# Optimization experiments

Hardware: AMD Instinct MI355X
Metric: run time of the kernel (lower is better)

Reference implementation:

```python
import jax, jax.numpy as jnp
import numpy as np
import math

B, N, D, L, H, FF, T = 8, 256, 384, 6, 8, 1536, 4
Dh = D // H  # 48, divisible by 6 for 3D rotary
N_M1 = T + 1 + 2 * N  # learn tokens + state + hand + head
S = 2 * N_M1


def rotary_pe_3d(x, coords):
    # x: [B,H,S,Dh], coords: [B,S,3]. Split head dim into 3 axis chunks,
    # apply standard RoPE per axis using the continuous coordinate as position.
    dh = x.shape[-1]
    d = dh // 3
    half = d // 2
    inv_freq = 1.0 / (10000.0 ** (jnp.arange(half, dtype=x.dtype) / half))
    outs = []
    for a in range(3):
        xa = x[..., a * d:(a + 1) * d]
        ang = coords[..., a][:, None, :, None] * inv_freq  # [B,1,S,half]
        c, s = jnp.cos(ang), jnp.sin(ang)
        x1, x2 = xa[..., :half], xa[..., half:]
        outs.append(jnp.concatenate([x1 * c - x2 * s, x1 * s + x2 * c], axis=-1))
    return jnp.concatenate(outs, axis=-1)


def layernorm(x, g, b):
    m = jnp.mean(x, axis=-1, keepdims=True)
    v = jnp.var(x, axis=-1, keepdims=True)
    return (x - m) * jax.lax.rsqrt(v + 1e-5) * g + b


def transformer_layer(src, coords_src, mask, Wq, bq, Wk, bk, Wv, bv, Wo, bo, W1, b1, W2, b2, g1, be1, g2, be2):
    Bsz, Ss, _ = src.shape
    q = jnp.einsum('bsd,od->bso', src, Wq) + bq
    k = jnp.einsum('bsd,od->bso', src, Wk) + bk
    v = jnp.einsum('bsd,od->bso', src, Wv) + bv
    q = q.reshape(Bsz, Ss, H, Dh).transpose(0, 2, 1, 3)
    k = k.reshape(Bsz, Ss, H, Dh).transpose(0, 2, 1, 3)
    v = v.reshape(Bsz, Ss, H, Dh).transpose(0, 2, 1, 3)
    q = rotary_pe_3d(q, coords_src)
    k = rotary_pe_3d(k, coords_src)
    scores = jnp.einsum('bhqd,bhkd->bhqk', q, k) / math.sqrt(Dh)
    scores = jnp.where(mask[None, None, :, :], -jnp.inf, scores)
    attn = jnp.einsum('bhqk,bhkd->bhqd', jax.nn.softmax(scores, axis=-1), v)
    attn = attn.transpose(0, 2, 1, 3).reshape(Bsz, Ss, D)
    attn = jnp.einsum('bsd,od->bso', attn, Wo) + bo
    src2 = layernorm(src + attn, g1, be1)
    ff = jnp.einsum('bsf,of->bso', jax.nn.gelu(jnp.einsum('bsd,fd->bsf', src2, W1) + b1, approximate=False), W2) + b2
    return layernorm(src2 + ff, g2, be2)


def setup_inputs() -> dict:
    key = jax.random.key(0)
    ks = jax.random.split(key, 32)
    rnd = lambda i, shape, scale=1.0: (jax.random.normal(ks[i], shape, dtype=jnp.float32) * scale)
    inp = {
        'hand_token_t': rnd(0, (B, N, D)),
        'head_token_t': rnd(1, (B, N, D)),
        'hand_token_m1': rnd(2, (B, N, D)),
        'head_token_m1': rnd(3, (B, N, D)),
        'coords_hand_t': rnd(4, (B, N, 3)),
        'coords_head_t': rnd(5, (B, N, 3)),
        'coords_hand_m1': rnd(6, (B, N, 3)),
        'coords_head_m1': rnd(7, (B, N, 3)),
        'state_t': rnd(8, (B, D)),
        'state_m1': rnd(9, (B, D)),
        'trans_head_t': rnd(10, (B, 3)),
        'trans_head_m1': rnd(11, (B, 3)),
        'tokens_m1': rnd(12, (1, T, D), 0.02),
        'tokens_t': rnd(13, (1, T, D), 0.02),
        'Wq': rnd(14, (L, D, D), 0.02), 'bq': jnp.zeros((L, D), jnp.float32),
        'Wk': rnd(15, (L, D, D), 0.02), 'bk': jnp.zeros((L, D), jnp.float32),
        'Wv': rnd(16, (L, D, D), 0.02), 'bv': jnp.zeros((L, D), jnp.float32),
        'Wo': rnd(17, (L, D, D), 0.02), 'bo': jnp.zeros((L, D), jnp.float32),
        'W1': rnd(18, (L, FF, D), 0.02), 'b1': jnp.zeros((L, FF), jnp.float32),
        'W2': rnd(19, (L, D, FF), 0.02), 'b2': jnp.zeros((L, D), jnp.float32),
        'g1': jnp.ones((L, D), jnp.float32), 'be1': jnp.zeros((L, D), jnp.float32),
        'g2': jnp.ones((L, D), jnp.float32), 'be2': jnp.zeros((L, D), jnp.float32),
    }
    return inp


def reference(hand_token_t, head_token_t, hand_token_m1, head_token_m1,
              coords_hand_t, coords_head_t, coords_hand_m1, coords_head_m1,
              state_t, state_m1, trans_head_t, trans_head_m1,
              tokens_m1, tokens_t, Wq, bq, Wk, bk, Wv, bv, Wo, bo,
              W1, b1, W2, b2, g1, be1, g2, be2):
    # Build token sequence: [state_m1, hand_m1, head_m1, learn_m1, state_t, hand_t, head_t, learn_t]
    tok_m1 = jnp.broadcast_to(tokens_m1, (B, T, D))
    tok_t = jnp.broadcast_to(tokens_t, (B, T, D))
    coord_m1 = jnp.broadcast_to(trans_head_m1[:, None, :], (B, T, 3))
    coord_t = jnp.broadcast_to(trans_head_t[:, None, :], (B, T, 3))
    src = jnp.concatenate([
        state_m1[:, None, :], hand_token_m1, head_token_m1, tok_m1,
        state_t[:, None, :], hand_token_t, head_token_t, tok_t], axis=1)
    coords_src = jnp.concatenate([
        trans_head_m1[:, None, :], coords_hand_m1, coords_head_m1, coord_m1,
        trans_head_t[:, None, :], coords_hand_t, coords_head_t, coord_t], axis=1)
    # block-causal mask: m1 block cannot attend to t block
    mask = jnp.zeros((S, S), dtype=bool).at[:N_M1, N_M1:].set(True)
    for i in range(L):
        src = transformer_layer(src, coords_src, mask,
                                Wq[i], bq[i], Wk[i], bk[i], Wv[i], bv[i], Wo[i], bo[i],
                                W1[i], b1[i], W2[i], b2[i], g1[i], be1[i], g2[i], be2[i])
    return src[:, -T:, :]
```

## Files before the change

kernel.cpp:

```cpp
#include <hip/hip_runtime.h>
#include <hip/hip_bf16.h>
#include <math.h>

#define BB 8
#define NN 256
#define DD 384
#define LL 6
#define HH 8
#define FFD 1536
#define TT 4
#define DH 48
#define NM1 517
#define SS 1034
#define SSP 1088
#define MROWS (BB*SS)
#define NQKV 1152
#define QSCALE2 (0.14433756729740643f * 1.4426950408889634f)

typedef unsigned short u16;
typedef unsigned int u32;
typedef short bf8 __attribute__((ext_vector_type(8)));
typedef float f32x4 __attribute__((ext_vector_type(4)));

__device__ __forceinline__ u16 f2bf(float f) {
  __hip_bfloat16 h = __float2bfloat16(f);
  return *reinterpret_cast<u16*>(&h);
}
__device__ __forceinline__ float bf2f(u16 u) {
  __hip_bfloat16 h;
  *reinterpret_cast<u16*>(&h) = u;
  return __bfloat162float(h);
}
__device__ __forceinline__ float max3f(float a, float b, float c) {
  return fmaxf(fmaxf(a, b), c);
}
__device__ __forceinline__ void async16(void* lds, const void* g) {
  __builtin_amdgcn_global_load_lds(
      (const __attribute__((address_space(1))) unsigned int*)g,
      (__attribute__((address_space(3))) unsigned int*)lds, 16, 0, 0);
}

__global__ void build_src(const float* __restrict__ hand_t, const float* __restrict__ head_t,
                          const float* __restrict__ hand_m1, const float* __restrict__ head_m1,
                          const float* __restrict__ state_t, const float* __restrict__ state_m1,
                          const float* __restrict__ tok_m1, const float* __restrict__ tok_t,
                          float* __restrict__ src, u16* __restrict__ srcb) {
  int idx = blockIdx.x * 256 + threadIdx.x;
  if (idx >= BB * SS * DD) return;
  int d = idx % DD;
  int bs = idx / DD;
  int s = bs % SS;
  int b = bs / SS;
  float val;
  if (s == 0)               val = state_m1[b * DD + d];
  else if (s <= NN)         val = hand_m1[((size_t)(b * NN + (s - 1))) * DD + d];
  else if (s <= 2 * NN)     val = head_m1[((size_t)(b * NN + (s - 1 - NN))) * DD + d];
  else if (s <= 2 * NN + TT) val = tok_m1[(s - (2 * NN + 1)) * DD + d];
  else if (s == NM1)        val = state_t[b * DD + d];
  else if (s <= NM1 + NN)   val = hand_t[((size_t)(b * NN + (s - NM1 - 1))) * DD + d];
  else if (s <= NM1 + 2 * NN) val = head_t[((size_t)(b * NN + (s - NM1 - 1 - NN))) * DD + d];
  else                      val = tok_t[(s - (NM1 + 2 * NN + 1)) * DD + d];
  src[idx] = val;
  srcb[idx] = f2bf(val);
}

__global__ void build_coords(const float* __restrict__ c_hand_t, const float* __restrict__ c_head_t,
                             const float* __restrict__ c_hand_m1, const float* __restrict__ c_head_m1,
                             const float* __restrict__ tr_t, const float* __restrict__ tr_m1,
                             float* __restrict__ coords) {
  int idx = blockIdx.x * 256 + threadIdx.x;
  if (idx >= BB * SS * 3) return;
  int a = idx % 3;
  int bs = idx / 3;
  int s = bs % SS;
  int b = bs / SS;
  float val;
  if (s == 0)               val = tr_m1[b * 3 + a];
  else if (s <= NN)         val = c_hand_m1[(b * NN + (s - 1)) * 3 + a];
  else if (s <= 2 * NN)     val = c_head_m1[(b * NN + (s - 1 - NN)) * 3 + a];
  else if (s <= 2 * NN + TT) val = tr_m1[b * 3 + a];
  else if (s == NM1)        val = tr_t[b * 3 + a];
  else if (s <= NM1 + NN)   val = c_hand_t[(b * NN + (s - NM1 - 1)) * 3 + a];
  else if (s <= NM1 + 2 * NN) val = c_head_t[(b * NN + (s - NM1 - 1 - NN)) * 3 + a];
  else                      val = tr_t[b * 3 + a];
  coords[idx] = val;
}

__global__ void build_trig(const float* __restrict__ coords, float2* __restrict__ trig) {
  int idx = blockIdx.x * 256 + threadIdx.x;
  if (idx >= BB * SS * 24) return;
  int i = idx & 7;
  int axis = (idx >> 3) % 3;
  int bs = idx / 24;
  float cv = coords[bs * 3 + axis];
  float inv = expf(-(float)i * 1.1512925464970229f);
  float ang = cv * inv;
  trig[idx] = make_float2(cosf(ang), sinf(ang));
}

__global__ void cvt_bf(const float* __restrict__ in, u16* __restrict__ out, int n4) {
  int idx = blockIdx.x * 256 + threadIdx.x;
  if (idx >= n4) return;
  float4 v = reinterpret_cast<const float4*>(in)[idx];
  short4 o;
  o.x = (short)f2bf(v.x); o.y = (short)f2bf(v.y);
  o.z = (short)f2bf(v.z); o.w = (short)f2bf(v.w);
  reinterpret_cast<short4*>(out)[idx] = o;
}

__global__ void pack_qkv(const float* __restrict__ Wq, const float* __restrict__ Wk,
                         const float* __restrict__ Wv, u16* __restrict__ wqkv) {
  int idx = blockIdx.x * 256 + threadIdx.x;
  const int TOTAL = LL * NQKV * 96;
  if (idx >= TOTAL) return;
  int k4 = idx % 96;
  int n = (idx / 96) % NQKV;
  int l = idx / (96 * NQKV);
  int sel = n / 384, nn = n - sel * 384;
  const float* W = (sel == 0) ? Wq : ((sel == 1) ? Wk : Wv);
  float4 v = *reinterpret_cast<const float4*>(W + ((size_t)l * 384 + nn) * 384 + k4 * 4);
  short4 o;
  o.x = (short)f2bf(v.x); o.y = (short)f2bf(v.y);
  o.z = (short)f2bf(v.z); o.w = (short)f2bf(v.w);
  *reinterpret_cast<short4*>(wqkv + ((size_t)(l * NQKV + n) * 384 + k4 * 4)) = o;
}

__global__ void pack_bqkv(const float* __restrict__ bq, const float* __restrict__ bk,
                          const float* __restrict__ bv, float* __restrict__ bqkv) {
  int idx = blockIdx.x * 256 + threadIdx.x;
  if (idx >= LL * NQKV) return;
  int n = idx % NQKV, l = idx / NQKV;
  int sel = n / 384, nn = n - sel * 384;
  const float* Bp = (sel == 0) ? bq : ((sel == 1) ? bk : bv);
  bqkv[idx] = Bp[l * 384 + nn];
}

__global__ void pad_vt(u16* __restrict__ vt) {
  int idx = blockIdx.x * 256 + threadIdx.x;
  const int PADW = SSP - SS;
  if (idx >= 64 * DH * PADW) return;
  int c = idx % PADW;
  int rd = idx / PADW;
  vt[(size_t)rd * SSP + SS + c] = 0;
}

__global__ void pad_qk(u16* __restrict__ qh, u16* __restrict__ kh) {
  int idx = blockIdx.x * 256 + threadIdx.x;
  if (idx >= 64 * SS * 16) return;
  int c = idx & 15;
  int row = idx >> 4;
  qh[(size_t)row * 64 + 48 + c] = 0;
  kh[(size_t)row * 64 + 48 + c] = 0;
}

template <int EPI, int OUT, int Nc, int Kc>
__global__ __launch_bounds__(512) void gemm_as(
    const u16* __restrict__ Ab, const u16* __restrict__ Wb,
    const float* __restrict__ bias, const float2* __restrict__ trig,
    const float* __restrict__ Rf,
    float* __restrict__ Cf, u16* __restrict__ Cb,
    u16* __restrict__ Ck, u16* __restrict__ Cv) {
  constexpr int BUFSZ = 24576;
  constexpr int M = MROWS;
  constexpr int nxt = Nc >> 6;
  constexpr int Mt = (M + 127) >> 7;
  __shared__ __align__(16) char sm[2 * BUFSZ];
  const int tid = threadIdx.x;

  const int gL = blockIdx.x;
  const int x8 = gL & 7, jj = gL >> 3;
  const int mt_ = x8 * 9 + jj / nxt;
  if (mt_ >= Mt) return;
  const int bm = mt_ << 7, bn = (jj % nxt) << 6;

  const int lid = tid & 63, w = tid >> 6;
  const int wm = w >> 1, wn = w & 1;
  const int l15 = lid & 15, lg = lid >> 4;
  const int lr = lid >> 3, lu = lid & 7;
  const int swz = lu ^ lr;
  f32x4 acc[2][2] = {};

  auto stage = [&](int bsel, int k0) {
    char* base = sm + bsel * BUFSZ;
#pragma unroll
    for (int q = 0; q < 2; ++q) {
      int row = w * 16 + q * 8 + lr;
      int grow = bm + row; if (grow >= M) grow = M - 1;
      async16(base + w * 2048 + q * 1024, Ab + (size_t)grow * Kc + k0 + (swz << 3));
    }
    async16(base + 16384 + w * 1024, Wb + (size_t)(bn + w * 8 + lr) * Kc + k0 + (swz << 3));
  };

  stage(0, 0);
  int bs = 0;

#pragma unroll
  for (int k0 = 0; k0 < Kc; k0 += 64) {
    if (k0 + 64 < Kc) {
      stage(bs ^ 1, k0 + 64);
      asm volatile("s_waitcnt vmcnt(3)" ::: "memory");
    } else {
      asm volatile("s_waitcnt vmcnt(0)" ::: "memory");
    }
    __builtin_amdgcn_s_barrier();
    const char* base = sm + bs * BUFSZ;
    bf8 a[2][2], bfr[2][2];
#pragma unroll
    for (int kf = 0; kf < 2; ++kf) {
#pragma unroll
      for (int mt = 0; mt < 2; ++mt) {
        int row = wm * 32 + mt * 16 + l15;
        int off = ((row << 7) + (kf << 6) + (lg << 4)) ^ ((row & 7) << 4);
        a[kf][mt] = *reinterpret_cast<const bf8*>(base + off);
      }
#pragma unroll
      for (int nt = 0; nt < 2; ++nt) {
        int row = wn * 32 + nt * 16 + l15;
        int off = 16384 + (((row << 7) + (kf << 6) + (lg << 4)) ^ ((row & 7) << 4));
        bfr[kf][nt] = *reinterpret_cast<const bf8*>(base + off);
      }
    }
#pragma unroll
    for (int kf = 0; kf < 2; ++kf)
#pragma unroll
      for (int mt = 0; mt < 2; ++mt)
#pragma unroll
        for (int nt = 0; nt < 2; ++nt)
          acc[mt][nt] = __builtin_amdgcn_mfma_f32_16x16x32_bf16(a[kf][mt], bfr[kf][nt], acc[mt][nt], 0, 0, 0);
    asm volatile("s_waitcnt lgkmcnt(0)" ::: "memory");
    __builtin_amdgcn_s_barrier();
    bs ^= 1;
  }

  if constexpr (OUT != 2) {
#pragma unroll
    for (int nt = 0; nt < 2; ++nt) {
      const int n = bn + wn * 32 + nt * 16 + l15;
      const float bsv = bias[n];
#pragma unroll
      for (int mt = 0; mt < 2; ++mt) {
        const int m0 = bm + wm * 32 + mt * 16 + lg * 4;
#pragma unroll
        for (int r = 0; r < 4; ++r) {
          int m = m0 + r;
          if (m >= M) continue;
          float v = acc[mt][nt][r] + bsv;
          if (EPI == 1) v = 0.5f * v * (1.0f + erff(v * 0.70710678118654752f));
          if (OUT == 0) Cf[(size_t)m * Nc + n] = v + Rf[(size_t)m * Nc + n];
          else          Cb[(size_t)m * Nc + n] = f2bf(v);
        }
      }
    }
  } else {
    float* tile = (float*)sm;
#pragma unroll
    for (int nt = 0; nt < 2; ++nt) {
      const int nl = wn * 32 + nt * 16 + l15;
      const float bsv = bias[bn + nl];
#pragma unroll
      for (int mt = 0; mt < 2; ++mt) {
#pragma unroll
        for (int r = 0; r < 4; ++r) {
          int ml = wm * 32 + mt * 16 + lg * 4 + r;
          tile[ml * 65 + nl] = acc[mt][nt][r] + bsv;
        }
      }
    }
    __syncthreads();
    const int bnm = bn % 384;
    const int sel = bn / 384;
    if (sel < 2) {
      u16* Cqk = (sel == 0) ? Cb : Ck;
      const int d = lid;
      const int nn_ = bnm + d;
      const int hdiv = nn_ / 48, hrem = nn_ - hdiv * 48;
      const int axis = hrem >> 4, ii = hrem & 7;
      const bool hi = (hrem & 8) != 0;
      for (int si = 0; si < 16; ++si) {
        int row = w * 16 + si;
        int m = bm + row;
        if (m >= M) break;
        int bI = m / SS, s = m - bI * SS;
        float v = tile[row * 65 + d];
        float p = tile[row * 65 + (d ^ 8)];
        float2 t = trig[(size_t)(bI * SS + s) * 24 + axis * 8 + ii];
        float outv = hi ? (p * t.y + v * t.x) : (v * t.x - p * t.y);
        if (sel == 0) outv *= QSCALE2;
        Cqk[((size_t)(bI * HH + hdiv) * SS + s) * 64 + hrem] = f2bf(outv);
      }
    } else {
      const int srow = tid & 127, dq = tid >> 7;
      const int m = bm + srow;
      if (m < M) {
        int bI = m / SS, s = m - bI * SS;
        for (int di = 0; di < 16; ++di) {
          int d = dq * 16 + di;
          int nn_ = bnm + d;
          int hdiv = nn_ / 48, hrem = nn_ - hdiv * 48;
          Cv[((size_t)(bI * HH + hdiv) * DH + hrem) * SSP + s] = f2bf(tile[srow * 65 + d]);
        }
      }
    }
  }
}

__global__ __launch_bounds__(512) void attn_mfma(const u16* __restrict__ qh,
                                                 const u16* __restrict__ kh,
                                                 const u16* __restrict__ vt,
                                                 u16* __restrict__ outb,
                                                 float* __restrict__ scr0,
                                                 float* __restrict__ scr1) {
  __shared__ __align__(16) char sm[32768];
  const int tid = threadIdx.x;
  const int lid = tid & 63, w = tid >> 6;
  const int l15 = lid & 15, lg = lid >> 4;
  const int lr = lid >> 3, lu = lid & 7;
  const int swz8 = (lu ^ lr) << 3;

  const int f = blockIdx.x;
  const int low = f & 7, j = f >> 3;
  const int gi = j / 14, it = j - gi * 14;
  const int g = gi * 8 + low;
  const int h = g & 7, b = g >> 3;
  int qblk, c0, c1, part;
  if (it < 10) { qblk = 4 + (it >> 1); part = it & 1; c0 = part ? 9 : 0; c1 = part ? 17 : 9; }
  else         { qblk = it - 10;       part = -1;     c0 = 0;            c1 = 9; }
  const int bh = b * HH + h;
  const int q0w = qblk * 128 + w * 16;
  const u16* kbase = kh + (size_t)bh * SS * 64;
  const u16* vbase = vt + (size_t)bh * DH * SSP;

  bf8 qf[2];
  {
    int row = q0w + l15; if (row >= SS) row = SS - 1;
    const u16* qp_ = qh + ((size_t)bh * SS + row) * 64;
    qf[0] = *reinterpret_cast<const bf8*>(qp_ + lg * 8);
    qf[1] = *reinterpret_cast<const bf8*>(qp_ + 32 + lg * 8);
  }
  const int qrow = q0w + l15;

  float m_q = -1e30f, l_q = 0.f;
  f32x4 accO[3] = {};

  auto stage = [&](int bsel, int c) {
    const int j0 = c * 64;
    char* kb = sm + bsel * 16384;
    char* vb = kb + 8192;
    {
      int s = w * 8 + lr;
      int jt_ = s >> 4, lgs = (s >> 2) & 3, rr = s & 3;
      int p = ((jt_ >> 1) << 5) + (lgs << 3) + ((jt_ & 1) << 2) + rr;
      int jrow = j0 + p; if (jrow >= SS) jrow = SS - 1;
      async16(kb + w * 1024, kbase + (size_t)jrow * 64 + swz8);
    }
    {
      int vrow = w * 8 + lr; if (vrow >= DH) vrow = DH - 1;
      async16(vb + w * 1024, vbase + (size_t)vrow * SSP + j0 + swz8);
    }
  };

  stage(0, c0);
  __syncthreads();
  int bsel = 0;

  for (int c = c0; c < c1; ++c) {
    if (c + 1 < c1) {
      stage(bsel ^ 1, c + 1);
      asm volatile("s_waitcnt vmcnt(2)" ::: "memory");
    } else {
      asm volatile("s_waitcnt vmcnt(0)" ::: "memory");
    }
    __builtin_amdgcn_s_barrier();
    const int j0 = c * 64;
    const char* kb = sm + bsel * 16384;
    const char* vb = kb + 8192;

    f32x4 sv[4];
    __builtin_amdgcn_s_setprio(1);
#pragma unroll
    for (int jt = 0; jt < 4; ++jt) {
      int row = jt * 16 + l15;
      int off0 = ((row << 7) + (lg << 4)) ^ ((row & 7) << 4);
      int off1 = ((row << 7) + 64 + (lg << 4)) ^ ((row & 7) << 4);
      bf8 kb0 = *reinterpret_cast<const bf8*>(kb + off0);
      bf8 kb1 = *reinterpret_cast<const bf8*>(kb + off1);
      f32x4 z = {};
      z = __builtin_amdgcn_mfma_f32_16x16x32_bf16(kb0, qf[0], z, 0, 0, 0);
      z = __builtin_amdgcn_mfma_f32_16x16x32_bf16(kb1, qf[1], z, 0, 0, 0);
      sv[jt] = z;
    }
    __builtin_amdgcn_s_setprio(0);

    const bool domask = (c == 16) | ((q0w < NM1) & (c >= 8));
    if (domask) {
#pragma unroll
      for (int jt = 0; jt < 4; ++jt)
#pragma unroll
        for (int r = 0; r < 4; ++r) {
          int kabs = j0 + ((jt >> 1) << 5) + (lg << 3) + ((jt & 1) << 2) + r;
          if (kabs >= SS || (qrow < NM1 && kabs >= NM1)) sv[jt][r] = -1e30f;
        }
    }

    float mx = max3f(sv[0][0], sv[0][1], sv[0][2]);
    mx = max3f(mx, sv[0][3], sv[1][0]);
    mx = max3f(mx, sv[1][1], sv[1][2]);
    mx = max3f(mx, sv[1][3], sv[2][0]);
    mx = max3f(mx, sv[2][1], sv[2][2]);
    mx = max3f(mx, sv[2][3], sv[3][0]);
    mx = max3f(mx, sv[3][1], sv[3][2]);
    mx = fmaxf(mx, sv[3][3]);
    mx = fmaxf(mx, __shfl_xor(mx, 16));
    mx = fmaxf(mx, __shfl_xor(mx, 32));

    const bool skip = __all(mx <= m_q);
    const float mn = skip ? m_q : fmaxf(m_q, mx);

    float pv[4][4];
    float ps = 0.f;
#pragma unroll
    for (int jt = 0; jt < 4; ++jt)
#pragma unroll
      for (int r = 0; r < 4; ++r) {
        float p = __builtin_amdgcn_exp2f(sv[jt][r] - mn);
        pv[jt][r] = p;
        ps += p;
      }
    ps += __shfl_xor(ps, 16);
    ps += __shfl_xor(ps, 32);

    if (!skip) {
      float alpha = __builtin_amdgcn_exp2f(m_q - mn);
      l_q = l_q * alpha + ps;
      m_q = mn;
      const int lg4 = lg * 4;
      float a0 = __shfl(alpha, lg4);
      float a1 = __shfl(alpha, lg4 + 1);
      float a2 = __shfl(alpha, lg4 + 2);
      float a3 = __shfl(alpha, lg4 + 3);
#pragma unroll
      for (int dt = 0; dt < 3; ++dt) {
        accO[dt][0] *= a0; accO[dt][1] *= a1;
        accO[dt][2] *= a2; accO[dt][3] *= a3;
      }
    } else {
      l_q += ps;
    }

    bf8 pa[2];
#pragma unroll
    for (int jc = 0; jc < 2; ++jc) {
      u32 w0 = (u32)f2bf(pv[jc * 2][0])     | ((u32)f2bf(pv[jc * 2][1]) << 16);
      u32 w1 = (u32)f2bf(pv[jc * 2][2])     | ((u32)f2bf(pv[jc * 2][3]) << 16);
      u32 w2 = (u32)f2bf(pv[jc * 2 + 1][0]) | ((u32)f2bf(pv[jc * 2 + 1][1]) << 16);
      u32 w3 = (u32)f2bf(pv[jc * 2 + 1][2]) | ((u32)f2bf(pv[jc * 2 + 1][3]) << 16);
      uint4 t = make_uint4(w0, w1, w2, w3);
      pa[jc] = *reinterpret_cast<bf8*>(&t);
    }

    __builtin_amdgcn_s_setprio(1);
#pragma unroll
    for (int dt = 0; dt < 3; ++dt) {
      int row = dt * 16 + l15;
#pragma unroll
      for (int jc = 0; jc < 2; ++jc) {
        int off = ((row << 7) + (jc << 6) + (lg << 4)) ^ ((row & 7) << 4);
        bf8 vb8 = *reinterpret_cast<const bf8*>(vb + off);
        accO[dt] = __builtin_amdgcn_mfma_f32_16x16x32_bf16(pa[jc], vb8, accO[dt], 0, 0, 0);
      }
    }
    __builtin_amdgcn_s_setprio(0);
    asm volatile("s_waitcnt lgkmcnt(0)" ::: "memory");
    __builtin_amdgcn_s_barrier();
    bsel ^= 1;
  }

  const int lg4 = lg * 4;
  if (part < 0) {
    float linv = 1.0f / l_q;
    float il[4];
#pragma unroll
    for (int r = 0; r < 4; ++r) il[r] = __shfl(linv, lg4 + r);
#pragma unroll
    for (int r = 0; r < 4; ++r) {
      int q = q0w + lg4 + r;
      if (q >= SS) continue;
#pragma unroll
      for (int dt = 0; dt < 3; ++dt) {
        int d = dt * 16 + l15;
        outb[((size_t)(b * SS + q)) * DD + h * DH + d] = f2bf(accO[dt][r] * il[r]);
      }
    }
  } else {
    float* pb = (part == 0) ? scr0 : scr1;
    const size_t base2 = (size_t)(bh * 5 + (qblk - 4)) * (128 * 50);
#pragma unroll
    for (int r = 0; r < 4; ++r) {
      int qloc = w * 16 + lg4 + r;
#pragma unroll
      for (int dt = 0; dt < 3; ++dt)
        pb[base2 + (size_t)qloc * 50 + dt * 16 + l15] = accO[dt][r];
    }
    if (lg == 0) {
      int qloc = w * 16 + l15;
      pb[base2 + (size_t)qloc * 50 + 48] = m_q;
      pb[base2 + (size_t)qloc * 50 + 49] = l_q;
    }
  }
}

__global__ void attn_merge(const float* __restrict__ s1, const float* __restrict__ s2,
                           u16* __restrict__ outb) {
  int idx = blockIdx.x * 256 + threadIdx.x;
  if (idx >= 64 * 5 * 128 * 48) return;
  int d = idx % 48;
  int row = idx / 48;
  int qloc = row & 127;
  int slot = row >> 7;
  int bh = slot / 5, qi = slot - bh * 5;
  int q = (4 + qi) * 128 + qloc;
  if (q >= SS) return;
  size_t o1 = (size_t)slot * (128 * 50) + qloc * 50;
  float m1 = s1[o1 + 48], l1 = s1[o1 + 49];
  float m2 = s2[o1 + 48], l2 = s2[o1 + 49];
  float m = fmaxf(m1, m2);
  float a1 = __builtin_amdgcn_exp2f(m1 - m);
  float a2 = __builtin_amdgcn_exp2f(m2 - m);
  float l = l1 * a1 + l2 * a2;
  float o = (s1[o1 + d] * a1 + s2[o1 + d] * a2) / l;
  int b = bh >> 3, h = bh & 7;
  outb[((size_t)(b * SS + q)) * DD + h * DH + d] = f2bf(o);
}

__global__ __launch_bounds__(512) void add_ln(const float* __restrict__ a,
                                              const float* __restrict__ g,
                                              const float* __restrict__ be,
                                              float* __restrict__ out,
                                              u16* __restrict__ outb) {
  const int w = threadIdx.x >> 6, lane = threadIdx.x & 63;
  const int row = blockIdx.x * 8 + w;
  const size_t base = (size_t)row * DD;
  float x[6];
#pragma unroll
  for (int jj = 0; jj < 6; ++jj) x[jj] = a[base + lane + 64 * jj];
  float s = x[0] + x[1] + x[2] + x[3] + x[4] + x[5];
#pragma unroll
  for (int off = 32; off; off >>= 1) s += __shfl_xor(s, off);
  float mean = s * (1.0f / 384.0f);
  float dv[6], vs = 0.f;
#pragma unroll
  for (int jj = 0; jj < 6; ++jj) { dv[jj] = x[jj] - mean; vs += dv[jj] * dv[jj]; }
#pragma unroll
  for (int off = 32; off; off >>= 1) vs += __shfl_xor(vs, off);
  float rs = rsqrtf(vs * (1.0f / 384.0f) + 1e-5f);
#pragma unroll
  for (int jj = 0; jj < 6; ++jj) {
    int c = lane + 64 * jj;
    float o = dv[jj] * rs * g[c] + be[c];
    out[base + c] = o;
    outb[base + c] = f2bf(o);
  }
}

__global__ void copy_out(const float* __restrict__ src, float* __restrict__ out) {
  int idx = blockIdx.x * 256 + threadIdx.x;
  if (idx >= BB * TT * DD) return;
  int d = idx % DD;
  int bt = idx / DD;
  int t = bt % TT;
  int b = bt / TT;
  out[idx] = src[((size_t)b * SS + (SS - TT) + t) * DD + d];
}

extern "C" void kernel_launch(void* const* d_in, const int* in_sizes, int n_in,
                              void* d_out, int out_size, void* d_ws, size_t ws_size,
                              hipStream_t stream) {
  const float* hand_t    = (const float*)d_in[0];
  const float* head_t    = (const float*)d_in[1];
  const float* hand_m1   = (const float*)d_in[2];
  const float* head_m1   = (const float*)d_in[3];
  const float* c_hand_t  = (const float*)d_in[4];
  const float* c_head_t  = (const float*)d_in[5];
  const float* c_hand_m1 = (const float*)d_in[6];
  const float* c_head_m1 = (const float*)d_in[7];
  const float* state_t   = (const float*)d_in[8];
  const float* state_m1  = (const float*)d_in[9];
  const float* tr_t      = (const float*)d_in[10];
  const float* tr_m1     = (const float*)d_in[11];
  const float* tok_m1    = (const float*)d_in[12];
  const float* tok_t     = (const float*)d_in[13];
  const float* Wq = (const float*)d_in[14];
  const float* bq = (const float*)d_in[15];
  const float* Wk = (const float*)d_in[16];
  const float* bk = (const float*)d_in[17];
  const float* Wv = (const float*)d_in[18];
  const float* bv = (const float*)d_in[19];
  const float* Wo = (const float*)d_in[20];
  const float* bo = (const float*)d_in[21];
  const float* W1 = (const float*)d_in[22];
  const float* b1 = (const float*)d_in[23];
  const float* W2 = (const float*)d_in[24];
  const float* b2 = (const float*)d_in[25];
  const float* g1 = (const float*)d_in[26];
  const float* be1 = (const float*)d_in[27];
  const float* g2 = (const float*)d_in[28];
  const float* be2 = (const float*)d_in[29];

  const size_t SRC_N = (size_t)BB * SS * DD;
  float* src    = (float*)d_ws;
  float* src2   = src + SRC_N;
  float* bufB   = src2 + SRC_N;
  float* coords = bufB + SRC_N;
  float* bqkv   = coords + (size_t)BB * SS * 3;
  float2* trig  = (float2*)(bqkv + (size_t)LL * NQKV);
  u16* srcb  = (u16*)(trig + (size_t)BB * SS * 24);
  u16* src2b = srcb + SRC_N;
  u16* attnb = src2b + SRC_N;
  u16* qh  = attnb + SRC_N;
  const size_t QH_N = (size_t)BB * HH * SS * 64;
  u16* khb = qh + QH_N;
  u16* vtb = khb + QH_N;
  u16* hbf = vtb + (size_t)64 * DH * SSP;
  u16* wqkv_b = hbf + (size_t)MROWS * FFD;
  const size_t WD = (size_t)LL * DD * DD;
  const size_t WF = (size_t)LL * FFD * DD;
  u16* wo_bf = wqkv_b + (size_t)LL * NQKV * 384;
  u16* w1_bf = wo_bf + WD;
  u16* w2_bf = w1_bf + WF;

  dim3 blk(256);
  dim3 blk512(512);

  build_src<<<(BB * SS * DD + 255) / 256, blk, 0, stream>>>(
      hand_t, head_t, hand_m1, head_m1, state_t, state_m1, tok_m1, tok_t, src, srcb);
  build_coords<<<(BB * SS * 3 + 255) / 256, blk, 0, stream>>>(
      c_hand_t, c_head_t, c_hand_m1, c_head_m1, tr_t, tr_m1, coords);
  build_trig<<<(BB * SS * 24 + 255) / 256, blk, 0, stream>>>(coords, trig);
  pack_qkv<<<(LL * NQKV * 96 + 255) / 256, blk, 0, stream>>>(Wq, Wk, Wv, wqkv_b);
  pack_bqkv<<<(LL * NQKV + 255) / 256, blk, 0, stream>>>(bq, bk, bv, bqkv);
  cvt_bf<<<(int)(WD / 4 + 255) / 256, blk, 0, stream>>>(Wo, wo_bf, (int)(WD / 4));
  cvt_bf<<<(int)(WF / 4 + 255) / 256, blk, 0, stream>>>(W1, w1_bf, (int)(WF / 4));
  cvt_bf<<<(int)(WF / 4 + 255) / 256, blk, 0, stream>>>(W2, w2_bf, (int)(WF / 4));
  pad_vt<<<(64 * DH * (SSP - SS) + 255) / 256, blk, 0, stream>>>(vtb);
  pad_qk<<<(64 * SS * 16 + 255) / 256, blk, 0, stream>>>(qh, khb);

  dim3 gqkv(18 * 72);
  dim3 gwo(6 * 72);
  dim3 gf1(24 * 72);
  dim3 gf2(6 * 72);
  dim3 gattn(14 * 8 * 8);
  dim3 gmrg((64 * 5 * 128 * 48 + 255) / 256);

  for (int l = 0; l < LL; ++l) {
    const u16* Wqkv_l = wqkv_b + (size_t)l * NQKV * 384;
    const u16* Wo_l = wo_bf + (size_t)l * DD * DD;
    const u16* W1_l = w1_bf + (size_t)l * FFD * DD;
    const u16* W2_l = w2_bf + (size_t)l * DD * FFD;

    gemm_as<0, 2, NQKV, DD><<<gqkv, blk512, 0, stream>>>(
        srcb, Wqkv_l, bqkv + l * NQKV, trig, nullptr, nullptr, qh, khb, vtb);
    attn_mfma<<<gattn, blk512, 0, stream>>>(qh, khb, vtb, attnb, src2, bufB);
    attn_merge<<<gmrg, blk, 0, stream>>>(src2, bufB, attnb);
    gemm_as<0, 0, DD, DD><<<gwo, blk512, 0, stream>>>(
        attnb, Wo_l, bo + l * DD, nullptr, src, bufB, nullptr, nullptr, nullptr);
    add_ln<<<MROWS / 8, blk512, 0, stream>>>(bufB, g1 + l * DD, be1 + l * DD, src2, src2b);
    gemm_as<1, 1, FFD, DD><<<gf1, blk512, 0, stream>>>(
        src2b, W1_l, b1 + l * FFD, nullptr, nullptr, nullptr, hbf, nullptr, nullptr);
    gemm_as<0, 0, DD, FFD><<<gf2, blk512, 0, stream>>>(
        hbf, W2_l, b2 + l * DD, nullptr, src2, bufB, nullptr, nullptr, nullptr);
    add_ln<<<MROWS / 8, blk512, 0, stream>>>(bufB, g2 + l * DD, be2 + l * DD, src, srcb);
  }
  copy_out<<<(BB * TT * DD + 255) / 256, blk, 0, stream>>>(src, (float*)d_out);
}
```

Measured before the change: 906.2 us.

## Enlarge GEMM M-tile to 256 rows and drop split-KV attention merge

The GEMM kernel now computes 256x64 output tiles instead of 128x64. Each wave holds four M-fragments, so every loaded B fragment is reused more often and fewer blocks are launched, at the cost of more registers and 80KB of LDS per block. Separately, the attention kernel no longer splits the long query blocks into two KV halves with a separate merge kernel. Each block now walks all KV chunks itself, which removes the scratch writes and one launch per layer but makes block work uneven (9 vs 17 chunks) and leaves fewer blocks.

```diff
diff --git a/kernel.cpp b/kernel.cpp
--- a/kernel.cpp
+++ b/kernel.cpp
@@ -154,41 +154,41 @@
 }
 
 template <int EPI, int OUT, int Nc, int Kc>
-__global__ __launch_bounds__(512) void gemm_as(
+__global__ __launch_bounds__(512, 4) void gemm_as(
     const u16* __restrict__ Ab, const u16* __restrict__ Wb,
     const float* __restrict__ bias, const float2* __restrict__ trig,
     const float* __restrict__ Rf,
     float* __restrict__ Cf, u16* __restrict__ Cb,
     u16* __restrict__ Ck, u16* __restrict__ Cv) {
-  constexpr int BUFSZ = 24576;
+  constexpr int BUFSZ = 40960;
   constexpr int M = MROWS;
   constexpr int nxt = Nc >> 6;
-  constexpr int Mt = (M + 127) >> 7;
+  constexpr int Mt = (M + 255) >> 8;
   __shared__ __align__(16) char sm[2 * BUFSZ];
   const int tid = threadIdx.x;
 
   const int gL = blockIdx.x;
   const int x8 = gL & 7, jj = gL >> 3;
-  const int mt_ = x8 * 9 + jj / nxt;
+  const int mt_ = x8 * 5 + jj / nxt;
   if (mt_ >= Mt) return;
-  const int bm = mt_ << 7, bn = (jj % nxt) << 6;
+  const int bm = mt_ << 8, bn = (jj % nxt) << 6;
 
   const int lid = tid & 63, w = tid >> 6;
   const int wm = w >> 1, wn = w & 1;
   const int l15 = lid & 15, lg = lid >> 4;
   const int lr = lid >> 3, lu = lid & 7;
   const int swz = lu ^ lr;
-  f32x4 acc[2][2] = {};
+  f32x4 acc[4][2] = {};
 
   auto stage = [&](int bsel, int k0) {
     char* base = sm + bsel * BUFSZ;
 #pragma unroll
-    for (int q = 0; q < 2; ++q) {
-      int row = w * 16 + q * 8 + lr;
+    for (int q = 0; q < 4; ++q) {
+      int row = w * 32 + q * 8 + lr;
       int grow = bm + row; if (grow >= M) grow = M - 1;
-      async16(base + w * 2048 + q * 1024, Ab + (size_t)grow * Kc + k0 + (swz << 3));
-    }
-    async16(base + 16384 + w * 1024, Wb + (size_t)(bn + w * 8 + lr) * Kc + k0 + (swz << 3));
+      async16(base + w * 4096 + q * 1024, Ab + (size_t)grow * Kc + k0 + (swz << 3));
+    }
+    async16(base + 32768 + w * 1024, Wb + (size_t)(bn + w * 8 + lr) * Kc + k0 + (swz << 3));
   };
 
   stage(0, 0);
@@ -198,32 +198,32 @@
   for (int k0 = 0; k0 < Kc; k0 += 64) {
     if (k0 + 64 < Kc) {
       stage(bs ^ 1, k0 + 64);
-      asm volatile("s_waitcnt vmcnt(3)" ::: "memory");
+      asm volatile("s_waitcnt vmcnt(5)" ::: "memory");
     } else {
       asm volatile("s_waitcnt vmcnt(0)" ::: "memory");
     }
     __builtin_amdgcn_s_barrier();
     const char* base = sm + bs * BUFSZ;
-    bf8 a[2][2], bfr[2][2];
+    bf8 a[2][4], bfr[2][2];
 #pragma unroll
     for (int kf = 0; kf < 2; ++kf) {
 #pragma unroll
-      for (int mt = 0; mt < 2; ++mt) {
-        int row = wm * 32 + mt * 16 + l15;
+      for (int mt = 0; mt < 4; ++mt) {
+        int row = wm * 64 + mt * 16 + l15;
         int off = ((row << 7) + (kf << 6) + (lg << 4)) ^ ((row & 7) << 4);
         a[kf][mt] = *reinterpret_cast<const bf8*>(base + off);
       }
 #pragma unroll
       for (int nt = 0; nt < 2; ++nt) {
         int row = wn * 32 + nt * 16 + l15;
-        int off = 16384 + (((row << 7) + (kf << 6) + (lg << 4)) ^ ((row & 7) << 4));
+        int off = 32768 + (((row << 7) + (kf << 6) + (lg << 4)) ^ ((row & 7) << 4));
         bfr[kf][nt] = *reinterpret_cast<const bf8*>(base + off);
       }
     }
 #pragma unroll
     for (int kf = 0; kf < 2; ++kf)
 #pragma unroll
-      for (int mt = 0; mt < 2; ++mt)
+      for (int mt = 0; mt < 4; ++mt)
 #pragma unroll
         for (int nt = 0; nt < 2; ++nt)
           acc[mt][nt] = __builtin_amdgcn_mfma_f32_16x16x32_bf16(a[kf][mt], bfr[kf][nt], acc[mt][nt], 0, 0, 0);
@@ -238,8 +238,8 @@
       const int n = bn + wn * 32 + nt * 16 + l15;
       const float bsv = bias[n];
 #pragma unroll
-      for (int mt = 0; mt < 2; ++mt) {
-        const int m0 = bm + wm * 32 + mt * 16 + lg * 4;
+      for (int mt = 0; mt < 4; ++mt) {
+        const int m0 = bm + wm * 64 + mt * 16 + lg * 4;
 #pragma unroll
         for (int r = 0; r < 4; ++r) {
           int m = m0 + r;
@@ -258,10 +258,10 @@
       const int nl = wn * 32 + nt * 16 + l15;
       const float bsv = bias[bn + nl];
 #pragma unroll
-      for (int mt = 0; mt < 2; ++mt) {
+      for (int mt = 0; mt < 4; ++mt) {
 #pragma unroll
         for (int r = 0; r < 4; ++r) {
-          int ml = wm * 32 + mt * 16 + lg * 4 + r;
+          int ml = wm * 64 + mt * 16 + lg * 4 + r;
           tile[ml * 65 + nl] = acc[mt][nt][r] + bsv;
         }
       }
@@ -276,8 +276,8 @@
       const int hdiv = nn_ / 48, hrem = nn_ - hdiv * 48;
       const int axis = hrem >> 4, ii = hrem & 7;
       const bool hi = (hrem & 8) != 0;
-      for (int si = 0; si < 16; ++si) {
-        int row = w * 16 + si;
+      for (int si = 0; si < 32; ++si) {
+        int row = w * 32 + si;
         int m = bm + row;
         if (m >= M) break;
         int bI = m / SS, s = m - bI * SS;
@@ -289,12 +289,12 @@
         Cqk[((size_t)(bI * HH + hdiv) * SS + s) * 64 + hrem] = f2bf(outv);
       }
     } else {
-      const int srow = tid & 127, dq = tid >> 7;
+      const int srow = tid & 255, dq = tid >> 8;
       const int m = bm + srow;
       if (m < M) {
         int bI = m / SS, s = m - bI * SS;
-        for (int di = 0; di < 16; ++di) {
-          int d = dq * 16 + di;
+        for (int di = 0; di < 32; ++di) {
+          int d = dq * 32 + di;
           int nn_ = bnm + d;
           int hdiv = nn_ / 48, hrem = nn_ - hdiv * 48;
           Cv[((size_t)(bI * HH + hdiv) * DH + hrem) * SSP + s] = f2bf(tile[srow * 65 + d]);
@@ -307,9 +307,7 @@
 __global__ __launch_bounds__(512) void attn_mfma(const u16* __restrict__ qh,
                                                  const u16* __restrict__ kh,
                                                  const u16* __restrict__ vt,
-                                                 u16* __restrict__ outb,
-                                                 float* __restrict__ scr0,
-                                                 float* __restrict__ scr1) {
+                                                 u16* __restrict__ outb) {
   __shared__ __align__(16) char sm[32768];
   const int tid = threadIdx.x;
   const int lid = tid & 63, w = tid >> 6;
@@ -319,12 +317,10 @@
 
   const int f = blockIdx.x;
   const int low = f & 7, j = f >> 3;
-  const int gi = j / 14, it = j - gi * 14;
+  const int gi = j / 9, qp = j - gi * 9;
   const int g = gi * 8 + low;
   const int h = g & 7, b = g >> 3;
-  int qblk, c0, c1, part;
-  if (it < 10) { qblk = 4 + (it >> 1); part = it & 1; c0 = part ? 9 : 0; c1 = part ? 17 : 9; }
-  else         { qblk = it - 10;       part = -1;     c0 = 0;            c1 = 9; }
+  const int qblk = (qp < 5) ? (4 + qp) : (qp - 5);
   const int bh = b * HH + h;
   const int q0w = qblk * 128 + w * 16;
   const u16* kbase = kh + (size_t)bh * SS * 64;
@@ -341,6 +337,8 @@
 
   float m_q = -1e30f, l_q = 0.f;
   f32x4 accO[3] = {};
+
+  const int nch = (qblk < 4) ? 9 : 17;
 
   auto stage = [&](int bsel, int c) {
     const int j0 = c * 64;
@@ -359,12 +357,12 @@
     }
   };
 
-  stage(0, c0);
+  stage(0, 0);
   __syncthreads();
   int bsel = 0;
 
-  for (int c = c0; c < c1; ++c) {
-    if (c + 1 < c1) {
+  for (int c = 0; c < nch; ++c) {
+    if (c + 1 < nch) {
       stage(bsel ^ 1, c + 1);
       asm volatile("s_waitcnt vmcnt(2)" ::: "memory");
     } else {
@@ -475,61 +473,21 @@
     bsel ^= 1;
   }
 
+  float linv = 1.0f / l_q;
   const int lg4 = lg * 4;
-  if (part < 0) {
-    float linv = 1.0f / l_q;
-    float il[4];
-#pragma unroll
-    for (int r = 0; r < 4; ++r) il[r] = __shfl(linv, lg4 + r);
-#pragma unroll
-    for (int r = 0; r < 4; ++r) {
-      int q = q0w + lg4 + r;
-      if (q >= SS) continue;
-#pragma unroll
-      for (int dt = 0; dt < 3; ++dt) {
-        int d = dt * 16 + l15;
-        outb[((size_t)(b * SS + q)) * DD + h * DH + d] = f2bf(accO[dt][r] * il[r]);
-      }
-    }
-  } else {
-    float* pb = (part == 0) ? scr0 : scr1;
-    const size_t base2 = (size_t)(bh * 5 + (qblk - 4)) * (128 * 50);
-#pragma unroll
-    for (int r = 0; r < 4; ++r) {
-      int qloc = w * 16 + lg4 + r;
-#pragma unroll
-      for (int dt = 0; dt < 3; ++dt)
-        pb[base2 + (size_t)qloc * 50 + dt * 16 + l15] = accO[dt][r];
-    }
-    if (lg == 0) {
-      int qloc = w * 16 + l15;
-      pb[base2 + (size_t)qloc * 50 + 48] = m_q;
-      pb[base2 + (size_t)qloc * 50 + 49] = l_q;
+  float il[4];
+#pragma unroll
+  for (int r = 0; r < 4; ++r) il[r] = __shfl(linv, lg4 + r);
+#pragma unroll
+  for (int r = 0; r < 4; ++r) {
+    int q = q0w + lg4 + r;
+    if (q >= SS) continue;
+#pragma unroll
+    for (int dt = 0; dt < 3; ++dt) {
+      int d = dt * 16 + l15;
+      outb[((size_t)(b * SS + q)) * DD + h * DH + d] = f2bf(accO[dt][r] * il[r]);
     }
   }
-}
-
-__global__ void attn_merge(const float* __restrict__ s1, const float* __restrict__ s2,
-                           u16* __restrict__ outb) {
-  int idx = blockIdx.x * 256 + threadIdx.x;
-  if (idx >= 64 * 5 * 128 * 48) return;
-  int d = idx % 48;
-  int row = idx / 48;
-  int qloc = row & 127;
-  int slot = row >> 7;
-  int bh = slot / 5, qi = slot - bh * 5;
-  int q = (4 + qi) * 128 + qloc;
-  if (q >= SS) return;
-  size_t o1 = (size_t)slot * (128 * 50) + qloc * 50;
-  float m1 = s1[o1 + 48], l1 = s1[o1 + 49];
-  float m2 = s2[o1 + 48], l2 = s2[o1 + 49];
-  float m = fmaxf(m1, m2);
-  float a1 = __builtin_amdgcn_exp2f(m1 - m);
-  float a2 = __builtin_amdgcn_exp2f(m2 - m);
-  float l = l1 * a1 + l2 * a2;
-  float o = (s1[o1 + d] * a1 + s2[o1 + d] * a2) / l;
-  int b = bh >> 3, h = bh & 7;
-  outb[((size_t)(b * SS + q)) * DD + h * DH + d] = f2bf(o);
 }
 
 __global__ __launch_bounds__(512) void add_ln(const float* __restrict__ a,
@@ -644,12 +602,11 @@
   pad_vt<<<(64 * DH * (SSP - SS) + 255) / 256, blk, 0, stream>>>(vtb);
   pad_qk<<<(64 * SS * 16 + 255) / 256, blk, 0, stream>>>(qh, khb);
 
-  dim3 gqkv(18 * 72);
-  dim3 gwo(6 * 72);
-  dim3 gf1(24 * 72);
-  dim3 gf2(6 * 72);
-  dim3 gattn(14 * 8 * 8);
-  dim3 gmrg((64 * 5 * 128 * 48 + 255) / 256);
+  dim3 gqkv(18 * 40);
+  dim3 gwo(6 * 40);
+  dim3 gf1(24 * 40);
+  dim3 gf2(6 * 40);
+  dim3 gattn(9 * 8 * 8);
 
   for (int l = 0; l < LL; ++l) {
     const u16* Wqkv_l = wqkv_b + (size_t)l * NQKV * 384;
@@ -659,8 +616,7 @@
 
     gemm_as<0, 2, NQKV, DD><<<gqkv, blk512, 0, stream>>>(
         srcb, Wqkv_l, bqkv + l * NQKV, trig, nullptr, nullptr, qh, khb, vtb);
-    attn_mfma<<<gattn, blk512, 0, stream>>>(qh, khb, vtb, attnb, src2, bufB);
-    attn_merge<<<gmrg, blk, 0, stream>>>(src2, bufB, attnb);
+    attn_mfma<<<gattn, blk512, 0, stream>>>(qh, khb, vtb, attnb);
     gemm_as<0, 0, DD, DD><<<gwo, blk512, 0, stream>>>(
         attnb, Wo_l, bo + l * DD, nullptr, src, bufB, nullptr, nullptr, nullptr);
     add_ln<<<MROWS / 8, blk512, 0, stream>>>(bufB, g1 + l * DD, be1 + l * DD, src2, src2b);
```

Result: slower. 980.0 us (+8.2%).
